# Optimization experiments

Measured on AMD Instinct MI355X. Metric: run time of the kernel, lower is better.

The kernel has to match this reference:

```python
import jax, jax.numpy as jnp
import numpy as np

N_NODES = 50000
N_EDGES = 800000
D = 128
BATCHSIZE = 64


def setup_inputs() -> dict:
    key = jax.random.key(0)
    k1, k2, k3, k4 = jax.random.split(key, 4)
    x = jax.random.normal(k1, (N_NODES, D), dtype=jnp.float32)
    eps = jnp.zeros((1,), dtype=jnp.float32)
    W_pred = jax.random.normal(k2, (D, D), dtype=jnp.float32) * (1.0 / np.sqrt(D))
    b_pred = jnp.zeros((D,), dtype=jnp.float32)
    edge_index = jax.random.randint(k3, (2, N_EDGES), 0, N_NODES, dtype=jnp.int64)
    batch = jnp.sort(jax.random.randint(k4, (N_NODES,), 0, BATCHSIZE, dtype=jnp.int64))
    return {"x": x, "eps": eps, "W_pred": W_pred, "b_pred": b_pred,
            "edge_index": edge_index, "batch": batch}


def reference(x, eps, W_pred, b_pred, edge_index, batch):
    src, dst = edge_index[0], edge_index[1]
    # spmm: sum of neighbor features for each destination node [N, D]
    agg = jax.ops.segment_sum(x[src], dst, num_segments=N_NODES)
    # eps-weighted self update (apply_func=None, norm=None)
    out = (1.0 + eps) * x + agg
    out = jax.nn.relu(out)  # activation='relu'
    # linear_prediction then per-graph scatter-add pooling
    pooled = out @ W_pred + b_pred  # [N, pooled_features]
    pooled2 = jax.ops.segment_sum(pooled, batch, num_segments=BATCHSIZE)  # [B, pooled]
    return out, pooled2
```

## Files before the change

kernel.cpp:

```cpp
#include <hip/hip_runtime.h>
#include <hip/hip_bf16.h>

#define N_NODES 50000
#define N_EDGES 800000
#define D 128
#define BATCHSIZE 64

#define CHUNK_BITS 7
#define CHUNK 128
#define NBUCKETS 391
#define NBUCKETS_PAD 392
#define CAP 2400

#define FB_TILE 4096
#define NTILES ((N_EDGES + FB_TILE - 1) / FB_TILE)
#define SLICES 8
#define SLICE_B 49
#define FB_THREADS 256
#define FB_GRID (NTILES * SLICES)

__device__ inline unsigned short f2bf(float f) {
    union { float f; unsigned u; } c; c.f = f;
    unsigned u = c.u;
    return (unsigned short)((u + 0x7fffu + ((u >> 16) & 1u)) >> 16);
}

__device__ inline float4 bf4_to_f4(uint2 u) {
    union { unsigned u; float f; } a, b, c, d;
    a.u = u.x << 16; b.u = u.x & 0xffff0000u;
    c.u = u.y << 16; d.u = u.y & 0xffff0000u;
    float4 r; r.x = a.f; r.y = b.f; r.z = c.f; r.w = d.f;
    return r;
}

__global__ __launch_bounds__(FB_THREADS) void bin_convert_kernel(
    const float* __restrict__ x,
    unsigned short* __restrict__ xb,
    const int* __restrict__ edge_index,
    int* __restrict__ gcur,
    int* __restrict__ bucket)
{
    __shared__ int hist[SLICE_B];
    __shared__ int gbase[SLICE_B];

    int t = threadIdx.x;
    int blk = blockIdx.x;

    if (xb != nullptr) {
        const int TOT4 = N_NODES * D / 4;
        for (int i = blk * FB_THREADS + t; i < TOT4; i += FB_GRID * FB_THREADS) {
            float4 v = *(const float4*)(x + (size_t)i * 4);
            uint2 pk;
            pk.x = (unsigned)f2bf(v.x) | ((unsigned)f2bf(v.y) << 16);
            pk.y = (unsigned)f2bf(v.z) | ((unsigned)f2bf(v.w) << 16);
            *(uint2*)(xb + (size_t)i * 4) = pk;
        }
    }

    int tile = blk >> 3;
    int sl   = blk & 7;
    int blo  = sl * SLICE_B;
    int bhi  = blo + SLICE_B; if (bhi > NBUCKETS) bhi = NBUCKETS;
    int nb   = bhi - blo;

    if (t < SLICE_B) hist[t] = 0;
    __syncthreads();

    int base = tile * FB_TILE;
    int lim = N_EDGES - base; if (lim > FB_TILE) lim = FB_TILE;

    int bkt[16];
    int pack[16];
#pragma unroll
    for (int j = 0; j < 4; ++j) {
        int rel = j * FB_THREADS + t;
        int e4 = rel * 4;
#pragma unroll
        for (int k = 0; k < 4; ++k) bkt[j * 4 + k] = -1;
        if (e4 < lim) {
            int4 s4 = *(const int4*)(edge_index + base + e4);
            int4 d4 = *(const int4*)(edge_index + N_EDGES + base + e4);
            int ss[4] = { s4.x, s4.y, s4.z, s4.w };
            int dd[4] = { d4.x, d4.y, d4.z, d4.w };
#pragma unroll
            for (int k = 0; k < 4; ++k) {
                int b = (dd[k] >> CHUNK_BITS) - blo;
                if ((unsigned)b < (unsigned)nb) {
                    bkt[j * 4 + k] = b;
                    pack[j * 4 + k] = (ss[k] << CHUNK_BITS) | (dd[k] & (CHUNK - 1));
                    atomicAdd(&hist[b], 1);
                }
            }
        }
    }
    __syncthreads();

    if (t < nb) {
        int c = hist[t];
        gbase[t] = c ? atomicAdd(&gcur[blo + t], c) : 0;
        hist[t] = 0;
    }
    __syncthreads();

#pragma unroll
    for (int k = 0; k < 16; ++k) {
        int b = bkt[k];
        if (b >= 0) {
            int pos = gbase[b] + atomicAdd(&hist[b], 1);
            if (pos < CAP) bucket[(size_t)(blo + b) * CAP + pos] = pack[k];
        }
    }
}

template<bool BF16>
__global__ __launch_bounds__(1024) void gather_sort_kernel(
    const float* __restrict__ x,
    const unsigned short* __restrict__ xb,
    const float* __restrict__ eps,
    const int* __restrict__ batch,
    const int* __restrict__ gcur,
    const int* __restrict__ bucket,
    float* __restrict__ out,
    float* __restrict__ S)
{
    __shared__ int   ebuf[CAP];
    __shared__ int   sorted[CAP];
    __shared__ int   hist[CHUNK];
    __shared__ int   offs[CHUNK + 1];
    __shared__ int   cursor[CHUNK];
    __shared__ float pool[8 * D];

    int c = blockIdx.x;
    int t = threadIdx.x;
    int lane = t & 31;
    int g = t >> 5;

    if (t < CHUNK) hist[t] = 0;
    for (int i = t; i < 8 * D; i += 1024) pool[i] = 0.0f;
    int cnt = gcur[c];
    if (cnt > CAP) cnt = CAP;
    __syncthreads();

    for (int i = t; i < cnt; i += 1024) {
        int p = bucket[(size_t)c * CAP + i];
        ebuf[i] = p;
        atomicAdd(&hist[p & (CHUNK - 1)], 1);
    }
    __syncthreads();

    if (t < 64) {
        int h0 = hist[2 * t], h1 = hist[2 * t + 1];
        int tot = h0 + h1;
        int incl = tot;
#pragma unroll
        for (int o = 1; o < 64; o <<= 1) {
            int y = __shfl_up(incl, o, 64);
            if (t >= o) incl += y;
        }
        int excl = incl - tot;
        offs[2 * t] = excl;          cursor[2 * t] = excl;
        offs[2 * t + 1] = excl + h0; cursor[2 * t + 1] = excl + h0;
        if (t == 63) offs[CHUNK] = incl;
    }
    __syncthreads();

    for (int i = t; i < cnt; i += 1024) {
        int p = ebuf[i];
        int pos = atomicAdd(&cursor[p & (CHUNK - 1)], 1);
        sorted[pos] = p >> CHUNK_BITS;
    }
    __syncthreads();

    int node0 = c << CHUNK_BITS;
    int base_b = batch[node0];
    float scale = 1.0f + eps[0];
    int dv_cur = -1;
    float4 ps = make_float4(0.f, 0.f, 0.f, 0.f);

#pragma unroll
    for (int k = 0; k < 4; ++k) {
        int d = 4 * g + k;
        int node = node0 + d;
        if (node >= N_NODES) break;
        int start = offs[d], end = offs[d + 1];
        float4 acc = make_float4(0.f, 0.f, 0.f, 0.f);
        int i = start;
        if (BF16) {
            for (; i + 4 <= end; i += 4) {
                int s0 = sorted[i], s1 = sorted[i + 1];
                int s2 = sorted[i + 2], s3 = sorted[i + 3];
                uint2 u0 = *(const uint2*)(xb + (size_t)s0 * D + lane * 4);
                uint2 u1 = *(const uint2*)(xb + (size_t)s1 * D + lane * 4);
                uint2 u2 = *(const uint2*)(xb + (size_t)s2 * D + lane * 4);
                uint2 u3 = *(const uint2*)(xb + (size_t)s3 * D + lane * 4);
                float4 v0 = bf4_to_f4(u0), v1 = bf4_to_f4(u1);
                float4 v2 = bf4_to_f4(u2), v3 = bf4_to_f4(u3);
                acc.x += (v0.x + v1.x) + (v2.x + v3.x);
                acc.y += (v0.y + v1.y) + (v2.y + v3.y);
                acc.z += (v0.z + v1.z) + (v2.z + v3.z);
                acc.w += (v0.w + v1.w) + (v2.w + v3.w);
            }
            for (; i < end; ++i) {
                uint2 u0 = *(const uint2*)(xb + (size_t)sorted[i] * D + lane * 4);
                float4 v0 = bf4_to_f4(u0);
                acc.x += v0.x; acc.y += v0.y; acc.z += v0.z; acc.w += v0.w;
            }
        } else {
            for (; i + 4 <= end; i += 4) {
                int s0 = sorted[i], s1 = sorted[i + 1];
                int s2 = sorted[i + 2], s3 = sorted[i + 3];
                const float4 v0 = *(const float4*)(x + (size_t)s0 * D + lane * 4);
                const float4 v1 = *(const float4*)(x + (size_t)s1 * D + lane * 4);
                const float4 v2 = *(const float4*)(x + (size_t)s2 * D + lane * 4);
                const float4 v3 = *(const float4*)(x + (size_t)s3 * D + lane * 4);
                acc.x += (v0.x + v1.x) + (v2.x + v3.x);
                acc.y += (v0.y + v1.y) + (v2.y + v3.y);
                acc.z += (v0.z + v1.z) + (v2.z + v3.z);
                acc.w += (v0.w + v1.w) + (v2.w + v3.w);
            }
            for (; i < end; ++i) {
                const float4 v0 = *(const float4*)(x + (size_t)sorted[i] * D + lane * 4);
                acc.x += v0.x; acc.y += v0.y; acc.z += v0.z; acc.w += v0.w;
            }
        }
        const float4 xv = *(const float4*)(x + (size_t)node * D + lane * 4);
        float4 o;
        o.x = fmaxf(fmaf(scale, xv.x, acc.x), 0.0f);
        o.y = fmaxf(fmaf(scale, xv.y, acc.y), 0.0f);
        o.z = fmaxf(fmaf(scale, xv.z, acc.z), 0.0f);
        o.w = fmaxf(fmaf(scale, xv.w, acc.w), 0.0f);
        *(float4*)(out + (size_t)node * D + lane * 4) = o;

        int dv = batch[node] - base_b;
        if (dv != dv_cur) {
            if (dv_cur >= 0) {
                if (dv_cur < 8) {
                    float* pp = &pool[dv_cur * D + lane * 4];
                    atomicAdd(pp + 0, ps.x); atomicAdd(pp + 1, ps.y);
                    atomicAdd(pp + 2, ps.z); atomicAdd(pp + 3, ps.w);
                } else {
                    float* sp = S + (size_t)(base_b + dv_cur) * D + lane * 4;
                    atomicAdd(sp + 0, ps.x); atomicAdd(sp + 1, ps.y);
                    atomicAdd(sp + 2, ps.z); atomicAdd(sp + 3, ps.w);
                }
            }
            ps = make_float4(0.f, 0.f, 0.f, 0.f);
            dv_cur = dv;
        }
        ps.x += o.x; ps.y += o.y; ps.z += o.z; ps.w += o.w;
    }
    if (dv_cur >= 0) {
        if (dv_cur < 8) {
            float* pp = &pool[dv_cur * D + lane * 4];
            atomicAdd(pp + 0, ps.x); atomicAdd(pp + 1, ps.y);
            atomicAdd(pp + 2, ps.z); atomicAdd(pp + 3, ps.w);
        } else {
            float* sp = S + (size_t)(base_b + dv_cur) * D + lane * 4;
            atomicAdd(sp + 0, ps.x); atomicAdd(sp + 1, ps.y);
            atomicAdd(sp + 2, ps.z); atomicAdd(sp + 3, ps.w);
        }
    }
    __syncthreads();

    int lastnode = node0 + CHUNK - 1;
    if (lastnode >= N_NODES) lastnode = N_NODES - 1;
    int used = batch[lastnode] - base_b + 1;
    if (used > 8) used = 8;
    for (int i = t; i < used * D; i += 1024) {
        atomicAdd(&S[(size_t)base_b * D + i], pool[i]);
    }
}

__device__ inline int lower_bound_dev(const int* __restrict__ a, int n, int key) {
    int lo = 0, hi = n;
    while (lo < hi) {
        int mid = (lo + hi) >> 1;
        if (a[mid] < key) lo = mid + 1; else hi = mid;
    }
    return lo;
}

__global__ void pool_gemm_kernel(const float* __restrict__ S,
                                 const int* __restrict__ batch,
                                 const float* __restrict__ W,
                                 const float* __restrict__ b_pred,
                                 float* __restrict__ pooled2) {
    int b = blockIdx.x;
    int j = threadIdx.x;
    int lo = lower_bound_dev(batch, N_NODES, b);
    int hi = lower_bound_dev(batch, N_NODES, b + 1);
    float acc = (float)(hi - lo) * b_pred[j];
    const float* srow = S + (size_t)b * D;
#pragma unroll 8
    for (int k = 0; k < D; ++k) {
        acc = fmaf(srow[k], W[(size_t)k * D + j], acc);
    }
    pooled2[(size_t)b * D + j] = acc;
}


__global__ void edge_scatter_kernel(const float* __restrict__ x,
                                    const int* __restrict__ edge_index,
                                    float* __restrict__ agg) {
    int tid = blockIdx.x * blockDim.x + threadIdx.x;
    int lane = tid & 31;
    int e = tid >> 5;
    if (e >= N_EDGES) return;
    int src = edge_index[e];
    int dst = edge_index[N_EDGES + e];
    const float4 v = *(const float4*)(x + (size_t)src * D + lane * 4);
    float* dp = agg + (size_t)dst * D + lane * 4;
    atomicAdd(dp + 0, v.x);
    atomicAdd(dp + 1, v.y);
    atomicAdd(dp + 2, v.z);
    atomicAdd(dp + 3, v.w);
}

__global__ void finalize_kernel(const float* __restrict__ x,
                                const float* __restrict__ eps,
                                const int* __restrict__ batch,
                                float* __restrict__ out,
                                float* __restrict__ Sf,
                                float* __restrict__ counts) {
    int tid = blockIdx.x * blockDim.x + threadIdx.x;
    int lane = tid & 31;
    int node = tid >> 5;
    if (node >= N_NODES) return;
    float scale = 1.0f + eps[0];
    const float4 xv = *(const float4*)(x + (size_t)node * D + lane * 4);
    float4 av = *(float4*)(out + (size_t)node * D + lane * 4);
    float4 o;
    o.x = fmaxf(fmaf(scale, xv.x, av.x), 0.0f);
    o.y = fmaxf(fmaf(scale, xv.y, av.y), 0.0f);
    o.z = fmaxf(fmaf(scale, xv.z, av.z), 0.0f);
    o.w = fmaxf(fmaf(scale, xv.w, av.w), 0.0f);
    *(float4*)(out + (size_t)node * D + lane * 4) = o;
    int b = batch[node];
    float* sp = Sf + (size_t)b * D + lane * 4;
    atomicAdd(sp + 0, o.x);
    atomicAdd(sp + 1, o.y);
    atomicAdd(sp + 2, o.z);
    atomicAdd(sp + 3, o.w);
    if (lane == 0) atomicAdd(counts + b, 1.0f);
}

__global__ void pool_gemm_fallback_kernel(const float* __restrict__ Sf,
                                          const float* __restrict__ counts,
                                          const float* __restrict__ W,
                                          const float* __restrict__ b_pred,
                                          float* __restrict__ pooled2) {
    int b = blockIdx.x;
    int j = threadIdx.x;
    float acc = counts[b] * b_pred[j];
    const float* srow = Sf + (size_t)b * D;
#pragma unroll 8
    for (int k = 0; k < D; ++k) {
        acc = fmaf(srow[k], W[(size_t)k * D + j], acc);
    }
    pooled2[(size_t)b * D + j] = acc;
}

extern "C" void kernel_launch(void* const* d_in, const int* in_sizes, int n_in,
                              void* d_out, int out_size, void* d_ws, size_t ws_size,
                              hipStream_t stream) {
    const float* x      = (const float*)d_in[0];
    const float* eps    = (const float*)d_in[1];
    const float* W_pred = (const float*)d_in[2];
    const float* b_pred = (const float*)d_in[3];
    const int*   eidx   = (const int*)d_in[4];
    const int*   batch  = (const int*)d_in[5];

    float* out     = (float*)d_out;
    float* pooled2 = (float*)d_out + (size_t)N_NODES * D;

    const size_t base_ints = (size_t)NBUCKETS_PAD + BATCHSIZE * D + (size_t)NBUCKETS * CAP;
    const size_t need_mid  = base_ints * 4;
    const size_t need_full = (base_ints + (size_t)N_NODES * D / 2) * 4;

    if (ws_size >= need_mid) {
        int*   gcur   = (int*)d_ws;
        float* S      = (float*)d_ws + NBUCKETS_PAD;
        int*   bucket = (int*)d_ws + NBUCKETS_PAD + BATCHSIZE * D;
        bool full = (ws_size >= need_full);
        unsigned short* xb = full ? (unsigned short*)((int*)d_ws + base_ints) : nullptr;

        hipMemsetAsync(d_ws, 0, (size_t)(NBUCKETS_PAD + BATCHSIZE * D) * 4, stream);

        bin_convert_kernel<<<FB_GRID, FB_THREADS, 0, stream>>>(x, xb, eidx, gcur, bucket);
        if (full) {
            gather_sort_kernel<true><<<NBUCKETS, 1024, 0, stream>>>(
                x, xb, eps, batch, gcur, bucket, out, S);
        } else {
            gather_sort_kernel<false><<<NBUCKETS, 1024, 0, stream>>>(
                x, (const unsigned short*)nullptr, eps, batch, gcur, bucket, out, S);
        }
        pool_gemm_kernel<<<BATCHSIZE, D, 0, stream>>>(S, batch, W_pred, b_pred, pooled2);
    } else {
        float* Sf      = (float*)d_ws;
        float* countsf = (float*)d_ws + BATCHSIZE * D;
        hipMemsetAsync(out, 0, (size_t)N_NODES * D * sizeof(float), stream);
        hipMemsetAsync(d_ws, 0, (BATCHSIZE * D + BATCHSIZE) * sizeof(float), stream);
        {
            long long total = (long long)N_EDGES * 32;
            int blocks = (int)((total + 255) / 256);
            edge_scatter_kernel<<<blocks, 256, 0, stream>>>(x, eidx, out);
        }
        {
            long long total = (long long)N_NODES * 32;
            int blocks = (int)((total + 255) / 256);
            finalize_kernel<<<blocks, 256, 0, stream>>>(x, eps, batch, out, Sf, countsf);
        }
        pool_gemm_fallback_kernel<<<BATCHSIZE, D, 0, stream>>>(Sf, countsf, W_pred, b_pred, pooled2);
    }
}
```

Before: 167.2 us.

## Fuse binning, gather and pooled GEMM into one cooperative kernel with grid syncs

Replaces the three-kernel sequence (bin/convert, gather-sort, pool GEMM) with a single cooperative launch of 391 blocks of 1024 threads. Grid-wide syncs separate the binning, gather and GEMM phases, which removes two kernel launch gaps. In exchange, the binning and bf16 conversion run on far fewer threads than the old 256-thread grid. If the cooperative launch fails, the code falls back to the original kernels.

Measured after the change: 277.9 us. 1.66x slower.

```diff
diff --git a/kernel.cpp b/kernel.cpp
--- a/kernel.cpp
+++ b/kernel.cpp
@@ -1,5 +1,8 @@
 #include <hip/hip_runtime.h>
 #include <hip/hip_bf16.h>
+#include <hip/hip_cooperative_groups.h>
+
+namespace cg = cooperative_groups;
 
 #define N_NODES 50000
 #define N_EDGES 800000
@@ -19,6 +22,8 @@
 #define FB_THREADS 256
 #define FB_GRID (NTILES * SLICES)
 
+#define COOP_EPB 2048
+
 __device__ inline unsigned short f2bf(float f) {
     union { float f; unsigned u; } c; c.f = f;
     unsigned u = c.u;
@@ -31,6 +36,258 @@
     c.u = u.y << 16; d.u = u.y & 0xffff0000u;
     float4 r; r.x = a.f; r.y = b.f; r.z = c.f; r.w = d.f;
     return r;
+}
+
+__device__ inline int lower_bound_dev(const int* __restrict__ a, int n, int key) {
+    int lo = 0, hi = n;
+    while (lo < hi) {
+        int mid = (lo + hi) >> 1;
+        if (a[mid] < key) lo = mid + 1; else hi = mid;
+    }
+    return lo;
+}
+
+struct SharedBufs {
+    int   ebuf[CAP];
+    int   sorted[CAP];
+    int   hist[CHUNK];
+    int   offs[CHUNK + 1];
+    int   cursor[CHUNK];
+    float pool[8 * D];
+};
+
+template<bool BF16>
+__device__ __forceinline__ void gather_phase(
+    SharedBufs& sb, int c, int t,
+    const float* __restrict__ x,
+    const unsigned short* __restrict__ xb,
+    float scale,
+    const int* __restrict__ batch,
+    const int* __restrict__ gcur,
+    const int* __restrict__ bucket,
+    float* __restrict__ out,
+    float* __restrict__ S)
+{
+    int lane = t & 31;
+    int g = t >> 5;
+
+    if (t < CHUNK) sb.hist[t] = 0;
+    for (int i = t; i < 8 * D; i += 1024) sb.pool[i] = 0.0f;
+    int cnt = gcur[c];
+    if (cnt > CAP) cnt = CAP;
+    __syncthreads();
+
+    for (int i = t; i < cnt; i += 1024) {
+        int p = bucket[(size_t)c * CAP + i];
+        sb.ebuf[i] = p;
+        atomicAdd(&sb.hist[p & (CHUNK - 1)], 1);
+    }
+    __syncthreads();
+
+    if (t < 64) {
+        int h0 = sb.hist[2 * t], h1 = sb.hist[2 * t + 1];
+        int tot = h0 + h1;
+        int incl = tot;
+#pragma unroll
+        for (int o = 1; o < 64; o <<= 1) {
+            int y = __shfl_up(incl, o, 64);
+            if (t >= o) incl += y;
+        }
+        int excl = incl - tot;
+        sb.offs[2 * t] = excl;          sb.cursor[2 * t] = excl;
+        sb.offs[2 * t + 1] = excl + h0; sb.cursor[2 * t + 1] = excl + h0;
+        if (t == 63) sb.offs[CHUNK] = incl;
+    }
+    __syncthreads();
+
+    for (int i = t; i < cnt; i += 1024) {
+        int p = sb.ebuf[i];
+        int pos = atomicAdd(&sb.cursor[p & (CHUNK - 1)], 1);
+        sb.sorted[pos] = p >> CHUNK_BITS;
+    }
+    __syncthreads();
+
+    int node0 = c << CHUNK_BITS;
+    int base_b = batch[node0];
+    int dv_cur = -1;
+    float4 ps = make_float4(0.f, 0.f, 0.f, 0.f);
+
+#pragma unroll
+    for (int k = 0; k < 4; ++k) {
+        int d = 4 * g + k;
+        int node = node0 + d;
+        if (node >= N_NODES) break;
+        int start = sb.offs[d], end = sb.offs[d + 1];
+        float4 acc = make_float4(0.f, 0.f, 0.f, 0.f);
+        int i = start;
+        if (BF16) {
+            for (; i + 4 <= end; i += 4) {
+                int s0 = sb.sorted[i], s1 = sb.sorted[i + 1];
+                int s2 = sb.sorted[i + 2], s3 = sb.sorted[i + 3];
+                uint2 u0 = *(const uint2*)(xb + (size_t)s0 * D + lane * 4);
+                uint2 u1 = *(const uint2*)(xb + (size_t)s1 * D + lane * 4);
+                uint2 u2 = *(const uint2*)(xb + (size_t)s2 * D + lane * 4);
+                uint2 u3 = *(const uint2*)(xb + (size_t)s3 * D + lane * 4);
+                float4 v0 = bf4_to_f4(u0), v1 = bf4_to_f4(u1);
+                float4 v2 = bf4_to_f4(u2), v3 = bf4_to_f4(u3);
+                acc.x += (v0.x + v1.x) + (v2.x + v3.x);
+                acc.y += (v0.y + v1.y) + (v2.y + v3.y);
+                acc.z += (v0.z + v1.z) + (v2.z + v3.z);
+                acc.w += (v0.w + v1.w) + (v2.w + v3.w);
+            }
+            for (; i < end; ++i) {
+                uint2 u0 = *(const uint2*)(xb + (size_t)sb.sorted[i] * D + lane * 4);
+                float4 v0 = bf4_to_f4(u0);
+                acc.x += v0.x; acc.y += v0.y; acc.z += v0.z; acc.w += v0.w;
+            }
+        } else {
+            for (; i + 4 <= end; i += 4) {
+                int s0 = sb.sorted[i], s1 = sb.sorted[i + 1];
+                int s2 = sb.sorted[i + 2], s3 = sb.sorted[i + 3];
+                const float4 v0 = *(const float4*)(x + (size_t)s0 * D + lane * 4);
+                const float4 v1 = *(const float4*)(x + (size_t)s1 * D + lane * 4);
+                const float4 v2 = *(const float4*)(x + (size_t)s2 * D + lane * 4);
+                const float4 v3 = *(const float4*)(x + (size_t)s3 * D + lane * 4);
+                acc.x += (v0.x + v1.x) + (v2.x + v3.x);
+                acc.y += (v0.y + v1.y) + (v2.y + v3.y);
+                acc.z += (v0.z + v1.z) + (v2.z + v3.z);
+                acc.w += (v0.w + v1.w) + (v2.w + v3.w);
+            }
+            for (; i < end; ++i) {
+                const float4 v0 = *(const float4*)(x + (size_t)sb.sorted[i] * D + lane * 4);
+                acc.x += v0.x; acc.y += v0.y; acc.z += v0.z; acc.w += v0.w;
+            }
+        }
+        const float4 xv = *(const float4*)(x + (size_t)node * D + lane * 4);
+        float4 o;
+        o.x = fmaxf(fmaf(scale, xv.x, acc.x), 0.0f);
+        o.y = fmaxf(fmaf(scale, xv.y, acc.y), 0.0f);
+        o.z = fmaxf(fmaf(scale, xv.z, acc.z), 0.0f);
+        o.w = fmaxf(fmaf(scale, xv.w, acc.w), 0.0f);
+        *(float4*)(out + (size_t)node * D + lane * 4) = o;
+
+        int dv = batch[node] - base_b;
+        if (dv != dv_cur) {
+            if (dv_cur >= 0) {
+                if (dv_cur < 8) {
+                    float* pp = &sb.pool[dv_cur * D + lane * 4];
+                    atomicAdd(pp + 0, ps.x); atomicAdd(pp + 1, ps.y);
+                    atomicAdd(pp + 2, ps.z); atomicAdd(pp + 3, ps.w);
+                } else {
+                    float* sp = S + (size_t)(base_b + dv_cur) * D + lane * 4;
+                    atomicAdd(sp + 0, ps.x); atomicAdd(sp + 1, ps.y);
+                    atomicAdd(sp + 2, ps.z); atomicAdd(sp + 3, ps.w);
+                }
+            }
+            ps = make_float4(0.f, 0.f, 0.f, 0.f);
+            dv_cur = dv;
+        }
+        ps.x += o.x; ps.y += o.y; ps.z += o.z; ps.w += o.w;
+    }
+    if (dv_cur >= 0) {
+        if (dv_cur < 8) {
+            float* pp = &sb.pool[dv_cur * D + lane * 4];
+            atomicAdd(pp + 0, ps.x); atomicAdd(pp + 1, ps.y);
+            atomicAdd(pp + 2, ps.z); atomicAdd(pp + 3, ps.w);
+        } else {
+            float* sp = S + (size_t)(base_b + dv_cur) * D + lane * 4;
+            atomicAdd(sp + 0, ps.x); atomicAdd(sp + 1, ps.y);
+            atomicAdd(sp + 2, ps.z); atomicAdd(sp + 3, ps.w);
+        }
+    }
+    __syncthreads();
+
+    int lastnode = node0 + CHUNK - 1;
+    if (lastnode >= N_NODES) lastnode = N_NODES - 1;
+    int used = batch[lastnode] - base_b + 1;
+    if (used > 8) used = 8;
+    for (int i = t; i < used * D; i += 1024) {
+        atomicAdd(&S[(size_t)base_b * D + i], sb.pool[i]);
+    }
+}
+
+__global__ __launch_bounds__(1024, 8) void fused_coop_kernel(
+    const float* __restrict__ x,
+    unsigned short* __restrict__ xb,
+    const int* __restrict__ edge_index,
+    const int* __restrict__ batch,
+    const float* __restrict__ eps,
+    const float* __restrict__ W,
+    const float* __restrict__ b_pred,
+    int* __restrict__ gcur,
+    int* __restrict__ bucket,
+    float* __restrict__ out,
+    float* __restrict__ S,
+    float* __restrict__ pooled2)
+{
+    __shared__ SharedBufs sb;
+    cg::grid_group grid = cg::this_grid();
+
+    int t = threadIdx.x;
+    int blk = blockIdx.x;
+
+    const int TOT4 = N_NODES * D / 4;
+    for (int i = blk * 1024 + t; i < TOT4; i += NBUCKETS * 1024) {
+        float4 v = *(const float4*)(x + (size_t)i * 4);
+        uint2 pk;
+        pk.x = (unsigned)f2bf(v.x) | ((unsigned)f2bf(v.y) << 16);
+        pk.y = (unsigned)f2bf(v.z) | ((unsigned)f2bf(v.w) << 16);
+        *(uint2*)(xb + (size_t)i * 4) = pk;
+    }
+
+    int* bhist  = sb.ebuf;
+    int* bgbase = sb.ebuf + NBUCKETS_PAD;
+    for (int i = t; i < NBUCKETS_PAD; i += 1024) bhist[i] = 0;
+    __syncthreads();
+
+    int base = blk * COOP_EPB;
+    int lim = N_EDGES - base; if (lim > COOP_EPB) lim = COOP_EPB; if (lim < 0) lim = 0;
+    int b0 = -1, b1 = -1, p0 = 0, p1 = 0;
+    int e = 2 * t;
+    if (e < lim) {
+        int2 s2 = *(const int2*)(edge_index + base + e);
+        int2 d2 = *(const int2*)(edge_index + N_EDGES + base + e);
+        b0 = d2.x >> CHUNK_BITS; p0 = (s2.x << CHUNK_BITS) | (d2.x & (CHUNK - 1));
+        b1 = d2.y >> CHUNK_BITS; p1 = (s2.y << CHUNK_BITS) | (d2.y & (CHUNK - 1));
+        atomicAdd(&bhist[b0], 1);
+        atomicAdd(&bhist[b1], 1);
+    }
+    __syncthreads();
+
+    for (int i = t; i < NBUCKETS; i += 1024) {
+        int c = bhist[i];
+        bgbase[i] = c ? atomicAdd(&gcur[i], c) : 0;
+    }
+    __syncthreads();
+    for (int i = t; i < NBUCKETS_PAD; i += 1024) bhist[i] = 0;
+    __syncthreads();
+
+    if (b0 >= 0) {
+        int pos = bgbase[b0] + atomicAdd(&bhist[b0], 1);
+        if (pos < CAP) bucket[(size_t)b0 * CAP + pos] = p0;
+        pos = bgbase[b1] + atomicAdd(&bhist[b1], 1);
+        if (pos < CAP) bucket[(size_t)b1 * CAP + pos] = p1;
+    }
+
+    grid.sync();
+
+    float scale = 1.0f + eps[0];
+    gather_phase<true>(sb, blk, t, x, xb, scale, batch, gcur, bucket, out, S);
+
+    grid.sync();
+
+    if (blk < BATCHSIZE && t < D) {
+        int b = blk, j = t;
+        int lo = lower_bound_dev(batch, N_NODES, b);
+        int hi = lower_bound_dev(batch, N_NODES, b + 1);
+        float acc = (float)(hi - lo) * b_pred[j];
+        const float* srow = S + (size_t)b * D;
+#pragma unroll 8
+        for (int k = 0; k < D; ++k) {
+            acc = fmaf(srow[k], W[(size_t)k * D + j], acc);
+        }
+        pooled2[(size_t)b * D + j] = acc;
+    }
 }
 
 __global__ __launch_bounds__(FB_THREADS) void bin_convert_kernel(
@@ -123,161 +380,9 @@
     float* __restrict__ out,
     float* __restrict__ S)
 {
-    __shared__ int   ebuf[CAP];
-    __shared__ int   sorted[CAP];
-    __shared__ int   hist[CHUNK];
-    __shared__ int   offs[CHUNK + 1];
-    __shared__ int   cursor[CHUNK];
-    __shared__ float pool[8 * D];
-
-    int c = blockIdx.x;
-    int t = threadIdx.x;
-    int lane = t & 31;
-    int g = t >> 5;
-
-    if (t < CHUNK) hist[t] = 0;
-    for (int i = t; i < 8 * D; i += 1024) pool[i] = 0.0f;
-    int cnt = gcur[c];
-    if (cnt > CAP) cnt = CAP;
-    __syncthreads();
-
-    for (int i = t; i < cnt; i += 1024) {
-        int p = bucket[(size_t)c * CAP + i];
-        ebuf[i] = p;
-        atomicAdd(&hist[p & (CHUNK - 1)], 1);
-    }
-    __syncthreads();
-
-    if (t < 64) {
-        int h0 = hist[2 * t], h1 = hist[2 * t + 1];
-        int tot = h0 + h1;
-        int incl = tot;
-#pragma unroll
-        for (int o = 1; o < 64; o <<= 1) {
-            int y = __shfl_up(incl, o, 64);
-            if (t >= o) incl += y;
-        }
-        int excl = incl - tot;
-        offs[2 * t] = excl;          cursor[2 * t] = excl;
-        offs[2 * t + 1] = excl + h0; cursor[2 * t + 1] = excl + h0;
-        if (t == 63) offs[CHUNK] = incl;
-    }
-    __syncthreads();
-
-    for (int i = t; i < cnt; i += 1024) {
-        int p = ebuf[i];
-        int pos = atomicAdd(&cursor[p & (CHUNK - 1)], 1);
-        sorted[pos] = p >> CHUNK_BITS;
-    }
-    __syncthreads();
-
-    int node0 = c << CHUNK_BITS;
-    int base_b = batch[node0];
+    __shared__ SharedBufs sb;
     float scale = 1.0f + eps[0];
-    int dv_cur = -1;
-    float4 ps = make_float4(0.f, 0.f, 0.f, 0.f);
-
-#pragma unroll
-    for (int k = 0; k < 4; ++k) {
-        int d = 4 * g + k;
-        int node = node0 + d;
-        if (node >= N_NODES) break;
-        int start = offs[d], end = offs[d + 1];
-        float4 acc = make_float4(0.f, 0.f, 0.f, 0.f);
-        int i = start;
-        if (BF16) {
-            for (; i + 4 <= end; i += 4) {
-                int s0 = sorted[i], s1 = sorted[i + 1];
-                int s2 = sorted[i + 2], s3 = sorted[i + 3];
-                uint2 u0 = *(const uint2*)(xb + (size_t)s0 * D + lane * 4);
-                uint2 u1 = *(const uint2*)(xb + (size_t)s1 * D + lane * 4);
-                uint2 u2 = *(const uint2*)(xb + (size_t)s2 * D + lane * 4);
-                uint2 u3 = *(const uint2*)(xb + (size_t)s3 * D + lane * 4);
-                float4 v0 = bf4_to_f4(u0), v1 = bf4_to_f4(u1);
-                float4 v2 = bf4_to_f4(u2), v3 = bf4_to_f4(u3);
-                acc.x += (v0.x + v1.x) + (v2.x + v3.x);
-                acc.y += (v0.y + v1.y) + (v2.y + v3.y);
-                acc.z += (v0.z + v1.z) + (v2.z + v3.z);
-                acc.w += (v0.w + v1.w) + (v2.w + v3.w);
-            }
-            for (; i < end; ++i) {
-                uint2 u0 = *(const uint2*)(xb + (size_t)sorted[i] * D + lane * 4);
-                float4 v0 = bf4_to_f4(u0);
-                acc.x += v0.x; acc.y += v0.y; acc.z += v0.z; acc.w += v0.w;
-            }
-        } else {
-            for (; i + 4 <= end; i += 4) {
-                int s0 = sorted[i], s1 = sorted[i + 1];
-                int s2 = sorted[i + 2], s3 = sorted[i + 3];
-                const float4 v0 = *(const float4*)(x + (size_t)s0 * D + lane * 4);
-                const float4 v1 = *(const float4*)(x + (size_t)s1 * D + lane * 4);
-                const float4 v2 = *(const float4*)(x + (size_t)s2 * D + lane * 4);
-                const float4 v3 = *(const float4*)(x + (size_t)s3 * D + lane * 4);
-                acc.x += (v0.x + v1.x) + (v2.x + v3.x);
-                acc.y += (v0.y + v1.y) + (v2.y + v3.y);
-                acc.z += (v0.z + v1.z) + (v2.z + v3.z);
-                acc.w += (v0.w + v1.w) + (v2.w + v3.w);
-            }
-            for (; i < end; ++i) {
-                const float4 v0 = *(const float4*)(x + (size_t)sorted[i] * D + lane * 4);
-                acc.x += v0.x; acc.y += v0.y; acc.z += v0.z; acc.w += v0.w;
-            }
-        }
-        const float4 xv = *(const float4*)(x + (size_t)node * D + lane * 4);
-        float4 o;
-        o.x = fmaxf(fmaf(scale, xv.x, acc.x), 0.0f);
-        o.y = fmaxf(fmaf(scale, xv.y, acc.y), 0.0f);
-        o.z = fmaxf(fmaf(scale, xv.z, acc.z), 0.0f);
-        o.w = fmaxf(fmaf(scale, xv.w, acc.w), 0.0f);
-        *(float4*)(out + (size_t)node * D + lane * 4) = o;
-
-        int dv = batch[node] - base_b;
-        if (dv != dv_cur) {
-            if (dv_cur >= 0) {
-                if (dv_cur < 8) {
-                    float* pp = &pool[dv_cur * D + lane * 4];
-                    atomicAdd(pp + 0, ps.x); atomicAdd(pp + 1, ps.y);
-                    atomicAdd(pp + 2, ps.z); atomicAdd(pp + 3, ps.w);
-                } else {
-                    float* sp = S + (size_t)(base_b + dv_cur) * D + lane * 4;
-                    atomicAdd(sp + 0, ps.x); atomicAdd(sp + 1, ps.y);
-                    atomicAdd(sp + 2, ps.z); atomicAdd(sp + 3, ps.w);
-                }
-            }
-            ps = make_float4(0.f, 0.f, 0.f, 0.f);
-            dv_cur = dv;
-        }
-        ps.x += o.x; ps.y += o.y; ps.z += o.z; ps.w += o.w;
-    }
-    if (dv_cur >= 0) {
-        if (dv_cur < 8) {
-            float* pp = &pool[dv_cur * D + lane * 4];
-            atomicAdd(pp + 0, ps.x); atomicAdd(pp + 1, ps.y);
-            atomicAdd(pp + 2, ps.z); atomicAdd(pp + 3, ps.w);
-        } else {
-            float* sp = S + (size_t)(base_b + dv_cur) * D + lane * 4;
-            atomicAdd(sp + 0, ps.x); atomicAdd(sp + 1, ps.y);
-            atomicAdd(sp + 2, ps.z); atomicAdd(sp + 3, ps.w);
-        }
-    }
-    __syncthreads();
-
-    int lastnode = node0 + CHUNK - 1;
-    if (lastnode >= N_NODES) lastnode = N_NODES - 1;
-    int used = batch[lastnode] - base_b + 1;
-    if (used > 8) used = 8;
-    for (int i = t; i < used * D; i += 1024) {
-        atomicAdd(&S[(size_t)base_b * D + i], pool[i]);
-    }
-}
-
-__device__ inline int lower_bound_dev(const int* __restrict__ a, int n, int key) {
-    int lo = 0, hi = n;
-    while (lo < hi) {
-        int mid = (lo + hi) >> 1;
-        if (a[mid] < key) lo = mid + 1; else hi = mid;
-    }
-    return lo;
+    gather_phase<BF16>(sb, blockIdx.x, threadIdx.x, x, xb, scale, batch, gcur, bucket, out, S);
 }
 
 __global__ void pool_gemm_kernel(const float* __restrict__ S,
@@ -386,15 +491,28 @@
 
         hipMemsetAsync(d_ws, 0, (size_t)(NBUCKETS_PAD + BATCHSIZE * D) * 4, stream);
 
-        bin_convert_kernel<<<FB_GRID, FB_THREADS, 0, stream>>>(x, xb, eidx, gcur, bucket);
+        bool done = false;
         if (full) {
-            gather_sort_kernel<true><<<NBUCKETS, 1024, 0, stream>>>(
-                x, xb, eps, batch, gcur, bucket, out, S);
-        } else {
-            gather_sort_kernel<false><<<NBUCKETS, 1024, 0, stream>>>(
-                x, (const unsigned short*)nullptr, eps, batch, gcur, bucket, out, S);
-        }
-        pool_gemm_kernel<<<BATCHSIZE, D, 0, stream>>>(S, batch, W_pred, b_pred, pooled2);
+            void* kargs[] = {
+                (void*)&x, (void*)&xb, (void*)&eidx, (void*)&batch, (void*)&eps,
+                (void*)&W_pred, (void*)&b_pred, (void*)&gcur, (void*)&bucket,
+                (void*)&out, (void*)&S, (void*)&pooled2
+            };
+            hipError_t err = hipLaunchCooperativeKernel(
+                (void*)fused_coop_kernel, dim3(NBUCKETS), dim3(1024), kargs, 0, stream);
+            done = (err == hipSuccess);
+        }
+        if (!done) {
+            bin_convert_kernel<<<FB_GRID, FB_THREADS, 0, stream>>>(x, xb, eidx, gcur, bucket);
+            if (full) {
+                gather_sort_kernel<true><<<NBUCKETS, 1024, 0, stream>>>(
+                    x, xb, eps, batch, gcur, bucket, out, S);
+            } else {
+                gather_sort_kernel<false><<<NBUCKETS, 1024, 0, stream>>>(
+                    x, (const unsigned short*)nullptr, eps, batch, gcur, bucket, out, S);
+            }
+            pool_gemm_kernel<<<BATCHSIZE, D, 0, stream>>>(S, batch, W_pred, b_pred, pooled2);
+        }
     } else {
         float* Sf      = (float*)d_ws;
         float* countsf = (float*)d_ws + BATCHSIZE * D;
```

## Fuse pooling GEMM into gather kernel and split buckets across two blocks

Applied to the files above, without the earlier changes.

Removes the separate pool_gemm kernel by having each gather block multiply its locally pooled rows by W_pred and atomically add the result straight into pooled2, with per-graph node counts kept in shared memory for the bias term. Each 128-node bucket is now handled by two 512-thread blocks, each owning half the destination nodes, which doubles the grid size. The binning pass uses 4 slices instead of 8 and also zeroes pooled2, so the S workspace memset goes away. The costs are that every block re-reads the whole bucket and filters it, each block runs a small GEMV over W, and pooled2 now receives more global atomics.

Result: faster. 157.3 us (-5.9%).

```diff
diff --git a/kernel.cpp b/kernel.cpp
--- a/kernel.cpp
+++ b/kernel.cpp
@@ -14,10 +14,13 @@
 
 #define FB_TILE 4096
 #define NTILES ((N_EDGES + FB_TILE - 1) / FB_TILE)
-#define SLICES 8
-#define SLICE_B 49
+#define SLICES 4
+#define SLICE_B 98
 #define FB_THREADS 256
 #define FB_GRID (NTILES * SLICES)
+
+#define GB_THREADS 512
+#define HCAP 1536
 
 __device__ inline unsigned short f2bf(float f) {
     union { float f; unsigned u; } c; c.f = f;
@@ -33,18 +36,31 @@
     return r;
 }
 
+__device__ inline int lower_bound_dev(const int* __restrict__ a, int n, int key) {
+    int lo = 0, hi = n;
+    while (lo < hi) {
+        int mid = (lo + hi) >> 1;
+        if (a[mid] < key) lo = mid + 1; else hi = mid;
+    }
+    return lo;
+}
+
 __global__ __launch_bounds__(FB_THREADS) void bin_convert_kernel(
     const float* __restrict__ x,
     unsigned short* __restrict__ xb,
     const int* __restrict__ edge_index,
     int* __restrict__ gcur,
-    int* __restrict__ bucket)
+    int* __restrict__ bucket,
+    float* __restrict__ pooled2)
 {
     __shared__ int hist[SLICE_B];
     __shared__ int gbase[SLICE_B];
 
     int t = threadIdx.x;
     int blk = blockIdx.x;
+
+    for (int i = blk * FB_THREADS + t; i < BATCHSIZE * D; i += FB_GRID * FB_THREADS)
+        pooled2[i] = 0.0f;
 
     if (xb != nullptr) {
         const int TOT4 = N_NODES * D / 4;
@@ -57,13 +73,13 @@
         }
     }
 
-    int tile = blk >> 3;
-    int sl   = blk & 7;
+    int tile = blk >> 2;
+    int sl   = blk & 3;
     int blo  = sl * SLICE_B;
     int bhi  = blo + SLICE_B; if (bhi > NBUCKETS) bhi = NBUCKETS;
     int nb   = bhi - blo;
 
-    if (t < SLICE_B) hist[t] = 0;
+    for (int i = t; i < SLICE_B; i += FB_THREADS) hist[i] = 0;
     __syncthreads();
 
     int base = tile * FB_TILE;
@@ -95,10 +111,10 @@
     }
     __syncthreads();
 
-    if (t < nb) {
-        int c = hist[t];
-        gbase[t] = c ? atomicAdd(&gcur[blo + t], c) : 0;
-        hist[t] = 0;
+    for (int i = t; i < nb; i += FB_THREADS) {
+        int c = hist[i];
+        gbase[i] = c ? atomicAdd(&gcur[blo + i], c) : 0;
+        hist[i] = 0;
     }
     __syncthreads();
 
@@ -113,66 +129,74 @@
 }
 
 template<bool BF16>
-__global__ __launch_bounds__(1024) void gather_sort_kernel(
+__global__ __launch_bounds__(GB_THREADS) void gather_kernel(
     const float* __restrict__ x,
     const unsigned short* __restrict__ xb,
     const float* __restrict__ eps,
     const int* __restrict__ batch,
     const int* __restrict__ gcur,
     const int* __restrict__ bucket,
+    const float* __restrict__ W,
+    const float* __restrict__ b_pred,
     float* __restrict__ out,
-    float* __restrict__ S)
+    float* __restrict__ pooled2)
 {
     __shared__ int   ebuf[CAP];
-    __shared__ int   sorted[CAP];
-    __shared__ int   hist[CHUNK];
-    __shared__ int   offs[CHUNK + 1];
-    __shared__ int   cursor[CHUNK];
+    __shared__ int   sorted[HCAP];
+    __shared__ int   hist[64];
+    __shared__ int   offs[65];
+    __shared__ int   cursor[64];
     __shared__ float pool[8 * D];
-
-    int c = blockIdx.x;
+    __shared__ int   pcount[8];
+
+    int blk = blockIdx.x;
+    int c = blk >> 1;
+    int h = blk & 1;
     int t = threadIdx.x;
     int lane = t & 31;
     int g = t >> 5;
 
-    if (t < CHUNK) hist[t] = 0;
-    for (int i = t; i < 8 * D; i += 1024) pool[i] = 0.0f;
+    if (t < 64) hist[t] = 0;
+    if (t < 8) pcount[t] = 0;
+    for (int i = t; i < 8 * D; i += GB_THREADS) pool[i] = 0.0f;
     int cnt = gcur[c];
     if (cnt > CAP) cnt = CAP;
     __syncthreads();
 
-    for (int i = t; i < cnt; i += 1024) {
+    for (int i = t; i < cnt; i += GB_THREADS) {
         int p = bucket[(size_t)c * CAP + i];
         ebuf[i] = p;
-        atomicAdd(&hist[p & (CHUNK - 1)], 1);
+        int dl = p & (CHUNK - 1);
+        if ((dl >> 6) == h) atomicAdd(&hist[dl & 63], 1);
     }
     __syncthreads();
 
     if (t < 64) {
-        int h0 = hist[2 * t], h1 = hist[2 * t + 1];
-        int tot = h0 + h1;
-        int incl = tot;
+        int v = hist[t];
+        int incl = v;
 #pragma unroll
         for (int o = 1; o < 64; o <<= 1) {
             int y = __shfl_up(incl, o, 64);
             if (t >= o) incl += y;
         }
-        int excl = incl - tot;
-        offs[2 * t] = excl;          cursor[2 * t] = excl;
-        offs[2 * t + 1] = excl + h0; cursor[2 * t + 1] = excl + h0;
-        if (t == 63) offs[CHUNK] = incl;
-    }
-    __syncthreads();
-
-    for (int i = t; i < cnt; i += 1024) {
+        offs[t] = incl - v;
+        cursor[t] = incl - v;
+        if (t == 63) offs[64] = incl;
+    }
+    __syncthreads();
+
+    for (int i = t; i < cnt; i += GB_THREADS) {
         int p = ebuf[i];
-        int pos = atomicAdd(&cursor[p & (CHUNK - 1)], 1);
-        sorted[pos] = p >> CHUNK_BITS;
-    }
-    __syncthreads();
-
-    int node0 = c << CHUNK_BITS;
-    int base_b = batch[node0];
+        int dl = p & (CHUNK - 1);
+        if ((dl >> 6) == h) {
+            int pos = atomicAdd(&cursor[dl & 63], 1);
+            if (pos < HCAP) sorted[pos] = p >> CHUNK_BITS;
+        }
+    }
+    __syncthreads();
+
+    int node0 = (c << CHUNK_BITS) + (h << 6);
+    int base_b = batch[node0 < N_NODES ? node0 : N_NODES - 1];
     float scale = 1.0f + eps[0];
     int dv_cur = -1;
     float4 ps = make_float4(0.f, 0.f, 0.f, 0.f);
@@ -183,6 +207,7 @@
         int node = node0 + d;
         if (node >= N_NODES) break;
         int start = offs[d], end = offs[d + 1];
+        if (end > HCAP) end = HCAP;
         float4 acc = make_float4(0.f, 0.f, 0.f, 0.f);
         int i = start;
         if (BF16) {
@@ -232,70 +257,42 @@
         *(float4*)(out + (size_t)node * D + lane * 4) = o;
 
         int dv = batch[node] - base_b;
-        if (dv != dv_cur) {
-            if (dv_cur >= 0) {
-                if (dv_cur < 8) {
+        if (dv < 8) {
+            if (dv != dv_cur) {
+                if (dv_cur >= 0) {
                     float* pp = &pool[dv_cur * D + lane * 4];
                     atomicAdd(pp + 0, ps.x); atomicAdd(pp + 1, ps.y);
                     atomicAdd(pp + 2, ps.z); atomicAdd(pp + 3, ps.w);
-                } else {
-                    float* sp = S + (size_t)(base_b + dv_cur) * D + lane * 4;
-                    atomicAdd(sp + 0, ps.x); atomicAdd(sp + 1, ps.y);
-                    atomicAdd(sp + 2, ps.z); atomicAdd(sp + 3, ps.w);
                 }
-            }
-            ps = make_float4(0.f, 0.f, 0.f, 0.f);
-            dv_cur = dv;
-        }
-        ps.x += o.x; ps.y += o.y; ps.z += o.z; ps.w += o.w;
+                ps = make_float4(0.f, 0.f, 0.f, 0.f);
+                dv_cur = dv;
+            }
+            ps.x += o.x; ps.y += o.y; ps.z += o.z; ps.w += o.w;
+            if (lane == 0) atomicAdd(&pcount[dv], 1);
+        }
     }
     if (dv_cur >= 0) {
-        if (dv_cur < 8) {
-            float* pp = &pool[dv_cur * D + lane * 4];
-            atomicAdd(pp + 0, ps.x); atomicAdd(pp + 1, ps.y);
-            atomicAdd(pp + 2, ps.z); atomicAdd(pp + 3, ps.w);
-        } else {
-            float* sp = S + (size_t)(base_b + dv_cur) * D + lane * 4;
-            atomicAdd(sp + 0, ps.x); atomicAdd(sp + 1, ps.y);
-            atomicAdd(sp + 2, ps.z); atomicAdd(sp + 3, ps.w);
-        }
-    }
-    __syncthreads();
-
-    int lastnode = node0 + CHUNK - 1;
+        float* pp = &pool[dv_cur * D + lane * 4];
+        atomicAdd(pp + 0, ps.x); atomicAdd(pp + 1, ps.y);
+        atomicAdd(pp + 2, ps.z); atomicAdd(pp + 3, ps.w);
+    }
+    __syncthreads();
+
+    int lastnode = node0 + 63;
     if (lastnode >= N_NODES) lastnode = N_NODES - 1;
     int used = batch[lastnode] - base_b + 1;
     if (used > 8) used = 8;
-    for (int i = t; i < used * D; i += 1024) {
-        atomicAdd(&S[(size_t)base_b * D + i], pool[i]);
-    }
-}
-
-__device__ inline int lower_bound_dev(const int* __restrict__ a, int n, int key) {
-    int lo = 0, hi = n;
-    while (lo < hi) {
-        int mid = (lo + hi) >> 1;
-        if (a[mid] < key) lo = mid + 1; else hi = mid;
-    }
-    return lo;
-}
-
-__global__ void pool_gemm_kernel(const float* __restrict__ S,
-                                 const int* __restrict__ batch,
-                                 const float* __restrict__ W,
-                                 const float* __restrict__ b_pred,
-                                 float* __restrict__ pooled2) {
-    int b = blockIdx.x;
-    int j = threadIdx.x;
-    int lo = lower_bound_dev(batch, N_NODES, b);
-    int hi = lower_bound_dev(batch, N_NODES, b + 1);
-    float acc = (float)(hi - lo) * b_pred[j];
-    const float* srow = S + (size_t)b * D;
+    if (t < D) {
+        for (int dv = 0; dv < used; ++dv) {
+            float acc = (float)pcount[dv] * b_pred[t];
+            const float* prow = &pool[dv * D];
 #pragma unroll 8
-    for (int k = 0; k < D; ++k) {
-        acc = fmaf(srow[k], W[(size_t)k * D + j], acc);
-    }
-    pooled2[(size_t)b * D + j] = acc;
+            for (int k = 0; k < D; ++k) {
+                acc = fmaf(prow[k], W[(size_t)k * D + t], acc);
+            }
+            atomicAdd(&pooled2[(size_t)(base_b + dv) * D + t], acc);
+        }
+    }
 }
 
 
@@ -373,28 +370,28 @@
     float* out     = (float*)d_out;
     float* pooled2 = (float*)d_out + (size_t)N_NODES * D;
 
-    const size_t base_ints = (size_t)NBUCKETS_PAD + BATCHSIZE * D + (size_t)NBUCKETS * CAP;
+    const size_t base_ints = (size_t)NBUCKETS_PAD + (size_t)NBUCKETS * CAP;
     const size_t need_mid  = base_ints * 4;
     const size_t need_full = (base_ints + (size_t)N_NODES * D / 2) * 4;
 
     if (ws_size >= need_mid) {
-        int*   gcur   = (int*)d_ws;
-        float* S      = (float*)d_ws + NBUCKETS_PAD;
-        int*   bucket = (int*)d_ws + NBUCKETS_PAD + BATCHSIZE * D;
+        int* gcur   = (int*)d_ws;
+        int* bucket = (int*)d_ws + NBUCKETS_PAD;
         bool full = (ws_size >= need_full);
         unsigned short* xb = full ? (unsigned short*)((int*)d_ws + base_ints) : nullptr;
 
-        hipMemsetAsync(d_ws, 0, (size_t)(NBUCKETS_PAD + BATCHSIZE * D) * 4, stream);
-
-        bin_convert_kernel<<<FB_GRID, FB_THREADS, 0, stream>>>(x, xb, eidx, gcur, bucket);
+        hipMemsetAsync(gcur, 0, (size_t)NBUCKETS_PAD * 4, stream);
+
+        bin_convert_kernel<<<FB_GRID, FB_THREADS, 0, stream>>>(
+            x, xb, eidx, gcur, bucket, pooled2);
         if (full) {
-            gather_sort_kernel<true><<<NBUCKETS, 1024, 0, stream>>>(
-                x, xb, eps, batch, gcur, bucket, out, S);
+            gather_kernel<true><<<NBUCKETS * 2, GB_THREADS, 0, stream>>>(
+                x, xb, eps, batch, gcur, bucket, W_pred, b_pred, out, pooled2);
         } else {
-            gather_sort_kernel<false><<<NBUCKETS, 1024, 0, stream>>>(
-                x, (const unsigned short*)nullptr, eps, batch, gcur, bucket, out, S);
-        }
-        pool_gemm_kernel<<<BATCHSIZE, D, 0, stream>>>(S, batch, W_pred, b_pred, pooled2);
+            gather_kernel<false><<<NBUCKETS * 2, GB_THREADS, 0, stream>>>(
+                x, (const unsigned short*)nullptr, eps, batch, gcur, bucket,
+                W_pred, b_pred, out, pooled2);
+        }
     } else {
         float* Sf      = (float*)d_ws;
         float* countsf = (float*)d_ws + BATCHSIZE * D;
```
